# Optimization experiments

Hardware: AMD Instinct MI355X
Metric: run time of the kernel (lower is better)

## Reference

```python
import jax, jax.numpy as jnp
import numpy as np

B, S, HID = 1, 2048, 7168
QLORA = 1536
NH = 32          # index_n_heads
HD = 128         # index_head_dim
ROPE = 64        # qk_rope_head_dim
TOPK = 512       # index_topk
EPS = 1e-6
NEG = -1e9       # finite mask value -> deterministic top-k (no -inf ties)


def _rope(x, cos, sin):
    # non-interleaved rotary: x [b,s,h,d]; cos/sin [s, d//2]
    half = x.shape[-1] // 2
    x1, x2 = x[..., :half], x[..., half:]
    c = cos[None, :, None, :]
    s = sin[None, :, None, :]
    return jnp.concatenate([x1 * c - x2 * s, x1 * s + x2 * c], axis=-1)


def setup_inputs() -> dict:
    key = jax.random.key(0)
    ks = jax.random.split(key, 8)
    x = jax.random.normal(ks[0], (B, S, HID), jnp.float32)
    qr = jax.random.normal(ks[1], (B, S, QLORA), jnp.float32)
    # rotary tables, theta=10000
    inv = 1.0 / (10000.0 ** (np.arange(0, ROPE, 2, dtype=np.float32) / ROPE))
    ang = np.arange(S, dtype=np.float32)[:, None] * inv[None, :]   # [S, ROPE//2]
    freqs_cos = jnp.asarray(np.cos(ang))
    freqs_sin = jnp.asarray(np.sin(ang))
    # causal additive mask [S, S], broadcasts over batch on [b,t,s]
    tri = jnp.tril(jnp.ones((S, S), jnp.bool_))
    mask = jnp.where(tri, 0.0, NEG).astype(jnp.float32)
    wq_b = jax.random.normal(ks[2], (QLORA, NH * HD), jnp.float32) / np.sqrt(QLORA)
    wk = jax.random.normal(ks[3], (HID, HD), jnp.float32) / np.sqrt(HID)
    k_norm_w = jnp.ones((HD,), jnp.float32)
    w_weights = jax.random.normal(ks[4], (HID, NH), jnp.float32) / np.sqrt(HID)
    return {"x": x, "qr": qr, "freqs_cos": freqs_cos, "freqs_sin": freqs_sin,
            "mask": mask, "wq_b": wq_b, "wk": wk, "k_norm_w": k_norm_w,
            "w_weights": w_weights}


def reference(x, qr, freqs_cos, freqs_sin, mask, wq_b, wk, k_norm_w, w_weights):
    b, s, _ = x.shape
    # queries
    q = (qr @ wq_b).reshape(b, s, NH, HD)
    q_pe, q_nope = q[..., :ROPE], q[..., ROPE:]
    q_pe = _rope(q_pe, freqs_cos, freqs_sin)
    q = jnp.concatenate([q_pe, q_nope], axis=-1)            # [b,s,NH,HD]
    # keys: project + RMSNorm + rope on first ROPE dims
    k = x @ wk                                              # [b,s,HD]
    var = jnp.mean(k * k, axis=-1, keepdims=True)
    k = k_norm_w * (k * jax.lax.rsqrt(var + EPS))
    k_pe, k_nope = k[..., :ROPE], k[..., ROPE:]
    k_pe = _rope(k_pe[:, :, None, :], freqs_cos, freqs_sin)[:, :, 0, :]
    k = jnp.concatenate([k_pe, k_nope], axis=-1)            # [b,s,HD]
    # per-head query weights
    weights = (x @ w_weights) * (NH ** -0.5) * (HD ** -0.5)  # [b,s,NH]
    # relu scores and per-head weighted reduction
    logits = jax.nn.relu(jnp.einsum('bthd,bsd->btsh', q, k))  # [b,t,s,NH]
    score = jnp.einsum('btsh,bth->bts', logits, weights) + mask
    # top-k token selection -> additive index mask
    topk_idx = jax.lax.top_k(score, min(TOPK, s))[1]          # [b,t,k]
    bi = jnp.arange(b)[:, None, None]
    ti = jnp.arange(s)[None, :, None]
    out = jnp.full((b, s, s), -jnp.inf, dtype=x.dtype)
    out = out.at[bi, ti, topk_idx].set(0.0)
    return out
```

## Files before the change

kernel.cpp:

```cpp
#include <hip/hip_runtime.h>
#include <hip/hip_bf16.h>
#include <math.h>

#define S_LEN 2048
#define HID   7168
#define QLORA 1536
#define NH    32
#define HD    128
#define T0    512
#define MROWS 1536
#define NEGV  -1000000000.0f
#define EPSV  1e-6f
#define NEG_FILL -3.0e38f
#define KSPLIT 16
#define KCHUNK 448

typedef __attribute__((ext_vector_type(8))) short bf16x8;
typedef __attribute__((ext_vector_type(4))) float f32x4;

__device__ __forceinline__ unsigned short f2bf(float x) {
    __hip_bfloat16 h = __float2bfloat16(x);
    union { __hip_bfloat16 h; unsigned short u; } cv; cv.h = h; return cv.u;
}
__device__ __forceinline__ float bf2f(short u) {
    return __uint_as_float(((unsigned)(unsigned short)u) << 16);
}
__device__ __forceinline__ void gload_lds16(const void* gsrc, void* ldst) {
    __builtin_amdgcn_global_load_lds(
        (const __attribute__((address_space(1))) void*)gsrc,
        (__attribute__((address_space(3))) void*)ldst,
        16, 0, 0);
}

__global__ __launch_bounds__(256) void transpose_wqb(
    const float* __restrict__ B, unsigned short* __restrict__ BT)
{
    __shared__ float tbuf[64][65];
    const int tid = threadIdx.x;
    const int n0 = blockIdx.x * 64;
    const int k0 = blockIdx.y * 64;
    {
        int r = tid >> 2, c0 = (tid & 3) * 16;
        const float* src = &B[(size_t)(k0 + r) * 4096 + n0 + c0];
        #pragma unroll
        for (int i = 0; i < 4; ++i) {
            float4 v = *(const float4*)(src + 4 * i);
            tbuf[r][c0 + 4 * i]     = v.x;
            tbuf[r][c0 + 4 * i + 1] = v.y;
            tbuf[r][c0 + 4 * i + 2] = v.z;
            tbuf[r][c0 + 4 * i + 3] = v.w;
        }
    }
    __syncthreads();
    {
        int nn = tid >> 2, ks = (tid & 3) * 16;
        bf16x8 p0, p1;
        #pragma unroll
        for (int j = 0; j < 8; ++j) {
            p0[j] = (short)f2bf(tbuf[ks + j][nn]);
            p1[j] = (short)f2bf(tbuf[ks + 8 + j][nn]);
        }
        unsigned short* dst = &BT[(size_t)(n0 + nn) * QLORA + k0 + ks];
        *(bf16x8*)dst       = p0;
        *(bf16x8*)(dst + 8) = p1;
    }
}

__global__ __launch_bounds__(256) void transpose_w(
    const float* __restrict__ wk, const float* __restrict__ ww,
    unsigned short* __restrict__ wbT)
{
    __shared__ float tbuf[64][33];
    const int tid = threadIdx.x;
    const int k0 = blockIdx.x * 64;
    const int nt = blockIdx.y;
    const float* src; int ld, nc0;
    if (nt < 4) { src = wk; ld = HD; nc0 = nt * 32; }
    else        { src = ww; ld = NH; nc0 = 0; }
    {
        int r = tid >> 2, c0 = (tid & 3) * 8;
        const float* sp = &src[(size_t)(k0 + r) * ld + nc0 + c0];
        #pragma unroll
        for (int i = 0; i < 2; ++i) {
            float4 v = *(const float4*)(sp + 4 * i);
            tbuf[r][c0 + 4 * i]     = v.x;
            tbuf[r][c0 + 4 * i + 1] = v.y;
            tbuf[r][c0 + 4 * i + 2] = v.z;
            tbuf[r][c0 + 4 * i + 3] = v.w;
        }
    }
    __syncthreads();
    {
        int nn = tid >> 3, ks = (tid & 7) * 8;
        bf16x8 p;
        #pragma unroll
        for (int j = 0; j < 8; ++j) p[j] = (short)f2bf(tbuf[ks + j][nn]);
        *(bf16x8*)&wbT[(size_t)(nt * 32 + nn) * HID + k0 + ks] = p;
    }
}

__global__ __launch_bounds__(256) void cast_qr(
    const float* __restrict__ qr, unsigned short* __restrict__ qrb)
{
    int idx = blockIdx.x * 256 + threadIdx.x;
    const float* src = qr + (size_t)T0 * QLORA + (size_t)idx * 8;
    float4 f0 = *(const float4*)src;
    float4 f1 = *(const float4*)(src + 4);
    bf16x8 p;
    p[0]=(short)f2bf(f0.x); p[1]=(short)f2bf(f0.y); p[2]=(short)f2bf(f0.z); p[3]=(short)f2bf(f0.w);
    p[4]=(short)f2bf(f1.x); p[5]=(short)f2bf(f1.y); p[6]=(short)f2bf(f1.z); p[7]=(short)f2bf(f1.w);
    *(bf16x8*)(qrb + (size_t)idx * 8) = p;
}

__global__ __launch_bounds__(256) void kw_gemm2(
    const float* __restrict__ x, const unsigned short* __restrict__ wbT,
    unsigned short* __restrict__ P)
{
    __shared__ char As[2][4096];
    __shared__ char Bs[2][10240];
    const int tid = threadIdx.x;
    const int bid = blockIdx.x;
    const int wg = (bid & 7) * 64 + (bid >> 3);
    const int kc = wg >> 5;
    const int m0 = (wg & 31) * 64;
    const int kbase = kc * KCHUNK;
    const int wv = tid >> 6, l = tid & 63, g = l >> 4, r15 = l & 15;
    const int ar = tid >> 2, asub = tid & 3;
    f32x4 acc[10] = {};
    float4 fa, fb;

#define LOAD_A(kt) do {                                                          \
        const float* ap = &x[(size_t)(m0 + ar) * HID + kbase + (kt) * 32 + asub * 8]; \
        fa = *(const float4*)ap;  fb = *(const float4*)(ap + 4);                 \
    } while (0)
#define WRITE_A(buf) do {                                                        \
        bf16x8 pk;                                                               \
        pk[0]=(short)f2bf(fa.x); pk[1]=(short)f2bf(fa.y);                        \
        pk[2]=(short)f2bf(fa.z); pk[3]=(short)f2bf(fa.w);                        \
        pk[4]=(short)f2bf(fb.x); pk[5]=(short)f2bf(fb.y);                        \
        pk[6]=(short)f2bf(fb.z); pk[7]=(short)f2bf(fb.w);                        \
        *(bf16x8*)(As[buf] + (ar << 6) + ((asub ^ ((ar >> 1) & 3)) << 4)) = pk;  \
    } while (0)
#define STAGE_B(buf, kt) do {                                                    \
        int k0_ = kbase + (kt) * 32;                                             \
        { int slot = (wv << 6) + l;                                              \
          int n_ = slot >> 2, sub_ = (slot & 3) ^ ((n_ >> 1) & 3);               \
          gload_lds16(wbT + (size_t)n_ * HID + k0_ + sub_ * 8,                   \
                      Bs[buf] + (wv << 10)); }                                   \
        { int slot = 256 + (wv << 6) + l;                                        \
          int n_ = slot >> 2, sub_ = (slot & 3) ^ ((n_ >> 1) & 3);               \
          gload_lds16(wbT + (size_t)n_ * HID + k0_ + sub_ * 8,                   \
                      Bs[buf] + 4096 + (wv << 10)); }                            \
        if (wv < 2) {                                                            \
          int slot = 512 + (wv << 6) + l;                                        \
          int n_ = slot >> 2, sub_ = (slot & 3) ^ ((n_ >> 1) & 3);               \
          gload_lds16(wbT + (size_t)n_ * HID + k0_ + sub_ * 8,                   \
                      Bs[buf] + 8192 + (wv << 10)); }                            \
    } while (0)

    LOAD_A(0);
    STAGE_B(0, 0);
    WRITE_A(0);
    __syncthreads();
    int cur = 0;
    for (int t = 0; t < 14; ++t) {
        if (t < 13) { LOAD_A(t + 1); STAGE_B(cur ^ 1, t + 1); }
        {
            char* Ab = As[cur];
            char* Bb = Bs[cur];
            int ra = (wv << 4) + r15;
            bf16x8 a = *(const bf16x8*)(Ab + (ra << 6) + ((g ^ ((ra >> 1) & 3)) << 4));
            #pragma unroll
            for (int fn = 0; fn < 10; ++fn) {
                int nb = (fn << 4) + r15;
                bf16x8 b = *(const bf16x8*)(Bb + (nb << 6) + ((g ^ ((nb >> 1) & 3)) << 4));
                acc[fn] = __builtin_amdgcn_mfma_f32_16x16x32_bf16(a, b, acc[fn], 0, 0, 0);
            }
        }
        if (t < 13) WRITE_A(cur ^ 1);
        __syncthreads();
        cur ^= 1;
    }
#undef LOAD_A
#undef WRITE_A
#undef STAGE_B
    #pragma unroll
    for (int fn = 0; fn < 10; ++fn)
        #pragma unroll
        for (int rr = 0; rr < 4; ++rr) {
            int row = m0 + (wv << 4) + (g << 2) + rr;
            P[((size_t)kc * S_LEN + row) * 160 + (fn << 4) + r15] = f2bf(acc[fn][rr]);
        }
}

__global__ __launch_bounds__(512) void kw_finish16(
    const unsigned short* __restrict__ P, const float* __restrict__ knw,
    const float* __restrict__ fcos, const float* __restrict__ fsin,
    unsigned short* __restrict__ Kf, float* __restrict__ W)
{
    __shared__ float res[16][160];
    __shared__ float rsq[16];
    const int tid = threadIdx.x;
    const int stile = blockIdx.x;
    const int row0 = stile * 16;
    const int r = tid >> 5, j = tid & 31;

    #pragma unroll
    for (int jj = 0; jj < 5; ++jj) {
        int c = j + 32 * jj;
        float s = 0.f;
        #pragma unroll
        for (int kc = 0; kc < KSPLIT; ++kc)
            s += bf2f((short)P[(size_t)(kc * S_LEN + row0 + r) * 160 + c]);
        res[r][c] = s;
    }
    __syncthreads();
    {
        float s2 = 0.f;
        #pragma unroll
        for (int cg = 0; cg < 4; ++cg) { float v = res[r][cg * 32 + j]; s2 += v * v; }
        #pragma unroll
        for (int off = 16; off > 0; off >>= 1) s2 += __shfl_xor(s2, off, 32);
        if (j == 0) rsq[r] = rsqrtf(s2 * (1.0f / 128.0f) + EPSV);
    }
    __syncthreads();
    {
        int rr = tid >> 5, h = tid & 31;
        W[(size_t)(row0 + rr) * NH + h] = res[rr][128 + h] * 0.015625f;
    }
    if (tid < 256) {
        int ks = tid >> 6, l = tid & 63;
        int row = l & 15, g = l >> 4;
        int t = row0 + row;
        float rs = rsq[row];
        bf16x8 pack;
        #pragma unroll
        for (int jj2 = 0; jj2 < 8; ++jj2) {
            int d = ks * 32 + 8 * g + jj2;
            float v;
            if (d < 32) {
                float a = res[row][d]      * rs * knw[d];
                float b = res[row][d + 32] * rs * knw[d + 32];
                v = a * fcos[(size_t)t * 32 + d] - b * fsin[(size_t)t * 32 + d];
            } else if (d < 64) {
                int jx = d - 32;
                float a = res[row][jx] * rs * knw[jx];
                float b = res[row][d]  * rs * knw[d];
                v = a * fsin[(size_t)t * 32 + jx] + b * fcos[(size_t)t * 32 + jx];
            } else {
                v = res[row][d] * rs * knw[d];
            }
            pack[jj2] = (short)f2bf(v);
        }
        *(bf16x8*)&Kf[(size_t)stile * 2048 + ks * 512 + l * 8] = pack;
    }
}

__global__ __launch_bounds__(256) void gemm_q2(
    const unsigned short* __restrict__ qrb, const unsigned short* __restrict__ wqbT,
    const float* __restrict__ fcos, const float* __restrict__ fsin,
    unsigned short* __restrict__ Qbu)
{
    __shared__ char lds[2][12288];
    const int tid = threadIdx.x;
    const int bid = blockIdx.x;
    const int wg = (bid & 7) * 96 + (bid >> 3);
    const int n0 = (wg / 24) * 128;
    const int m0 = (wg % 24) * 64;
    const int wv = tid >> 6, l = tid & 63, g = l >> 4, r15 = l & 15;
    const int lrow = l >> 2, lsub = l & 3;
    const int wm = wv >> 1, wn = wv & 1;
    f32x4 acc[2][4] = {};

#define STAGE_Q(buf, kt) do {                                                   \
        int k0_ = (kt) * 32;                                                    \
        { int row_ = wv * 16 + lrow; int gs_ = lsub ^ ((row_ >> 1) & 3);        \
          gload_lds16(qrb + (size_t)(m0 + row_) * QLORA + k0_ + gs_ * 8,        \
                      lds[buf] + (wv << 10)); }                                 \
        { int row_ = wv * 32 + lrow; int gs_ = lsub ^ ((row_ >> 1) & 3);        \
          gload_lds16(wqbT + (size_t)(n0 + row_) * QLORA + k0_ + gs_ * 8,       \
                      lds[buf] + 4096 + (wv << 11)); }                          \
        { int row_ = wv * 32 + 16 + lrow; int gs_ = lsub ^ ((row_ >> 1) & 3);   \
          gload_lds16(wqbT + (size_t)(n0 + row_) * QLORA + k0_ + gs_ * 8,       \
                      lds[buf] + 4096 + (wv << 11) + 1024); }                   \
    } while (0)

    STAGE_Q(0, 0);
    __syncthreads();
    int cur = 0;
    for (int t = 0; t < 48; ++t) {
        if (t + 1 < 48) STAGE_Q(cur ^ 1, t + 1);
        char* As = lds[cur];
        char* Bs = lds[cur] + 4096;
        bf16x8 a[2], b[4];
        #pragma unroll
        for (int fm = 0; fm < 2; ++fm) {
            int ra = wm * 32 + fm * 16 + r15;
            a[fm] = *(const bf16x8*)(As + (ra << 6) + ((g ^ ((ra >> 1) & 3)) << 4));
        }
        #pragma unroll
        for (int fn = 0; fn < 4; ++fn) {
            int nb = wn * 64 + fn * 16 + r15;
            b[fn] = *(const bf16x8*)(Bs + (nb << 6) + ((g ^ ((nb >> 1) & 3)) << 4));
        }
        #pragma unroll
        for (int fm = 0; fm < 2; ++fm)
            #pragma unroll
            for (int fn = 0; fn < 4; ++fn)
                acc[fm][fn] = __builtin_amdgcn_mfma_f32_16x16x32_bf16(a[fm], b[fn], acc[fm][fn], 0, 0, 0);
        __syncthreads();
        cur ^= 1;
    }
#undef STAGE_Q
    if (wn == 0) {
        #pragma unroll
        for (int fm = 0; fm < 2; ++fm)
            #pragma unroll
            for (int rr = 0; rr < 4; ++rr) {
                int t = T0 + m0 + wm * 32 + fm * 16 + 4 * g + rr;
                #pragma unroll
                for (int p = 0; p < 2; ++p) {
                    int jj = p * 16 + r15;
                    float c = fcos[(size_t)t * 32 + jj];
                    float s = fsin[(size_t)t * 32 + jj];
                    float a = acc[fm][p][rr], b = acc[fm][p + 2][rr];
                    acc[fm][p][rr]     = a * c - b * s;
                    acc[fm][p + 2][rr] = a * s + b * c;
                }
            }
    }
    #pragma unroll
    for (int fm = 0; fm < 2; ++fm)
        #pragma unroll
        for (int fn = 0; fn < 4; ++fn)
            #pragma unroll
            for (int rr = 0; rr < 4; ++rr) {
                int row = m0 + wm * 32 + fm * 16 + 4 * g + rr;
                int col = n0 + wn * 64 + fn * 16 + r15;
                Qbu[(size_t)row * 4096 + col] = f2bf(acc[fm][fn][rr]);
            }
}

__global__ __launch_bounds__(256, 2) void score_mfma2(
    const unsigned short* __restrict__ Qb, const unsigned short* __restrict__ Kf,
    const float* __restrict__ W, float* __restrict__ sc)
{
    __shared__ float ps[4][320];
    __shared__ float wl2[32][16];
    const int tid = threadIdx.x;
    const int tt  = 95 - blockIdx.x;
    const int sp  = blockIdx.y;
    const int t0  = T0 + 16 * tt;
    const int wv  = tid >> 6, l = tid & 63, g = l >> 4, r15 = l & 15;

    for (int i = tid; i < 512; i += 256) {
        int h = i >> 4, gg = (i >> 2) & 3, r = i & 3;
        wl2[h][gg * 4 + r] = W[(size_t)(t0 + 4 * gg + r) * NH + h];
    }
    bf16x8 qf[8][4];
    {
        const unsigned short* qbase = Qb + (size_t)(16 * tt + r15) * 4096 + g * 8;
        #pragma unroll
        for (int hh = 0; hh < 8; ++hh)
            #pragma unroll
            for (int ks = 0; ks < 4; ++ks)
                qf[hh][ks] = *(const bf16x8*)(qbase + (8 * wv + hh) * 128 + ks * 32);
    }
    __syncthreads();

    const int nst = 33 + tt;
    for (int stile = sp; stile < nst; stile += 4) {
        bf16x8 kf[4];
        #pragma unroll
        for (int ks = 0; ks < 4; ++ks)
            kf[ks] = *(const bf16x8*)&Kf[(size_t)stile * 2048 + ks * 512 + l * 8];
        f32x4 score = {0.f, 0.f, 0.f, 0.f};
        #pragma unroll
        for (int hh = 0; hh < 8; ++hh) {
            f32x4 acc = {0.f, 0.f, 0.f, 0.f};
            #pragma unroll
            for (int ks = 0; ks < 4; ++ks)
                acc = __builtin_amdgcn_mfma_f32_16x16x32_bf16(qf[hh][ks], kf[ks], acc, 0, 0, 0);
            f32x4 w4 = *(const f32x4*)&wl2[8 * wv + hh][g * 4];
            #pragma unroll
            for (int r = 0; r < 4; ++r)
                score[r] += fmaxf(acc[r], 0.f) * w4[r];
        }
        #pragma unroll
        for (int r = 0; r < 4; ++r) ps[wv][l * 5 + r] = score[r];
        __syncthreads();
        {
            float v = ((ps[0][l * 5 + wv] + ps[1][l * 5 + wv])
                       + ps[2][l * 5 + wv]) + ps[3][l * 5 + wv];
            int t = t0 + 4 * g + wv;
            int s = stile * 16 + r15;
            sc[(size_t)(t - T0) * S_LEN + s] = (s <= t) ? v : NEGV;
        }
        __syncthreads();
    }
}

__global__ __launch_bounds__(256) void topk_row(
    const float* __restrict__ sc, float* __restrict__ out)
{
    __shared__ float scl[S_LEN];
    __shared__ unsigned int hist[256];
    __shared__ unsigned int wtot[4];
    __shared__ unsigned int sh_prefix;
    __shared__ int sh_krem;
    const int tid = threadIdx.x;
    const int lane = tid & 63, wvi = tid >> 6;
    const int qrow = blockIdx.x;
    const int t = T0 + qrow;
    const float* srow = sc + (size_t)qrow * S_LEN;

    for (int i = tid; i < S_LEN; i += 256) {
        float v = srow[i];
        scl[i] = (i <= t) ? v : NEGV;
    }
    __syncthreads();
    unsigned int* u = (unsigned int*)scl;
    #pragma unroll
    for (int jj = 0; jj < 8; ++jj) {
        int i = tid * 8 + jj;
        unsigned int b = __float_as_uint(scl[i]);
        u[i] = (b & 0x80000000u) ? ~b : (b | 0x80000000u);
    }
    if (tid == 0) { sh_prefix = 0u; sh_krem = 512; }
    __syncthreads();

    #pragma unroll
    for (int pass = 0; pass < 4; ++pass) {
        const int shift = 24 - 8 * pass;
        hist[tid] = 0u;
        __syncthreads();
        unsigned int pfx = sh_prefix;
        #pragma unroll
        for (int jj = 0; jj < 8; ++jj) {
            unsigned int uv = u[tid * 8 + jj];
            bool ok = (pass == 0) || ((uv >> (shift + 8)) == (pfx >> (shift + 8)));
            if (ok) atomicAdd(&hist[(uv >> shift) & 255u], 1u);
        }
        __syncthreads();
        unsigned int v = hist[tid];
        unsigned int s = v;
        #pragma unroll
        for (int off = 1; off < 64; off <<= 1) {
            unsigned int t2 = __shfl_down(s, off, 64);
            if (lane + off < 64) s += t2;
        }
        if (lane == 0) wtot[wvi] = s;
        int krem = sh_krem;
        __syncthreads();
        unsigned int S = s;
        #pragma unroll
        for (int w = 0; w < 4; ++w)
            if (w > wvi) S += wtot[w];
        if ((int)S >= krem && (int)(S - v) < krem) {
            sh_krem = krem - (int)(S - v);
            sh_prefix = pfx | ((unsigned int)tid << shift);
        }
        __syncthreads();
    }

    const unsigned int uthr = sh_prefix;
    const int krem = sh_krem;
    int ec = 0;
    #pragma unroll
    for (int jj = 0; jj < 8; ++jj) ec += (u[tid * 8 + jj] == uthr) ? 1 : 0;
    unsigned int c = (unsigned int)ec;
    unsigned int p = c;
    #pragma unroll
    for (int off = 1; off < 64; off <<= 1) {
        unsigned int t2 = __shfl_up(p, off, 64);
        if (lane >= off) p += t2;
    }
    if (lane == 63) wtot[wvi] = p;
    __syncthreads();
    unsigned int add = 0;
    #pragma unroll
    for (int w = 0; w < 4; ++w)
        if (w < wvi) add += wtot[w];
    int base = (int)(p - c + add);

    float* orow = out + (size_t)t * S_LEN;
    float o[8];
    #pragma unroll
    for (int jj = 0; jj < 8; ++jj) {
        unsigned int uv = u[tid * 8 + jj];
        bool sel;
        if (uv > uthr) { sel = true; }
        else if (uv == uthr) { sel = (base < krem); base++; }
        else { sel = false; }
        o[jj] = sel ? 0.0f : NEG_FILL;
    }
    float4 o0 = {o[0], o[1], o[2], o[3]};
    float4 o1 = {o[4], o[5], o[6], o[7]};
    *(float4*)&orow[tid * 8]     = o0;
    *(float4*)&orow[tid * 8 + 4] = o1;
}

__global__ __launch_bounds__(256) void fill_low(float* __restrict__ out)
{
    int idx = blockIdx.x * 256 + threadIdx.x;
    if (idx >= (T0 * S_LEN) / 4) return;
    int col4 = idx & 511;
    float v = (col4 < 128) ? 0.0f : NEG_FILL;
    float4 o = {v, v, v, v};
    ((float4*)out)[idx] = o;
}

extern "C" void kernel_launch(void* const* d_in, const int* in_sizes, int n_in,
                              void* d_out, int out_size, void* d_ws, size_t ws_size,
                              hipStream_t stream)
{
    (void)in_sizes; (void)n_in; (void)out_size; (void)ws_size;
    const float* x    = (const float*)d_in[0];
    const float* qr   = (const float*)d_in[1];
    const float* fcos = (const float*)d_in[2];
    const float* fsin = (const float*)d_in[3];
    const float* wq_b = (const float*)d_in[5];
    const float* wk   = (const float*)d_in[6];
    const float* knw  = (const float*)d_in[7];
    const float* ww   = (const float*)d_in[8];
    float* out = (float*)d_out;
    char*  wsb = (char*)d_ws;

    unsigned short* Kf   = (unsigned short*)wsb;
    float*          W    = (float*)(wsb + 512 * 1024);
    char*           reg1 = wsb + 768 * 1024;
    char*           reg2 = reg1 + 12582912;
    unsigned short* wbT  = (unsigned short*)reg1;
    unsigned short* Qbu  = (unsigned short*)reg1;
    unsigned short* P    = (unsigned short*)reg2;
    unsigned short* wqbT = (unsigned short*)reg2;
    float*          sc   = (float*)reg2;
    unsigned short* qrb  = (unsigned short*)d_out;

    transpose_w   <<<dim3(112, 5), 256, 0, stream>>>(wk, ww, wbT);
    kw_gemm2      <<<512, 256,        0, stream>>>(x, wbT, P);
    kw_finish16   <<<128, 512,        0, stream>>>(P, knw, fcos, fsin, Kf, W);
    transpose_wqb <<<dim3(64, 24), 256, 0, stream>>>(wq_b, wqbT);
    cast_qr       <<<1152, 256,       0, stream>>>(qr, qrb);
    gemm_q2       <<<768, 256,        0, stream>>>(qrb, wqbT, fcos, fsin, Qbu);
    score_mfma2   <<<dim3(96, 4), 256,  0, stream>>>(Qbu, Kf, W, sc);
    topk_row      <<<MROWS, 256,      0, stream>>>(sc, out);
    fill_low      <<<(T0 * S_LEN / 4 + 255) / 256, 256, 0, stream>>>(out);
}
```

Measured before the change: 159.3 us.

## Split score kernel heads across 8 waves with K prefetch and double-buffered reduction

The score kernel now runs 512 threads per block, so each wave handles 4 heads instead of 8, which halves the Q fragment registers held per thread. K fragments for the next s-tile are prefetched while the current tile's MFMAs run. The partial-sum buffer is double-buffered so the trailing barrier can be dropped. In exchange the cross-wave reduction sums 8 partials instead of 4, and only half the waves do the final reduce and store.

Measured after the change: 156.0 us. 1.02x faster.

```diff
diff --git a/kernel.cpp b/kernel.cpp
--- a/kernel.cpp
+++ b/kernel.cpp
@@ -341,11 +341,11 @@
             }
 }
 
-__global__ __launch_bounds__(256, 2) void score_mfma2(
+__global__ __launch_bounds__(512, 2) void score_mfma3(
     const unsigned short* __restrict__ Qb, const unsigned short* __restrict__ Kf,
     const float* __restrict__ W, float* __restrict__ sc)
 {
-    __shared__ float ps[4][320];
+    __shared__ float ps[2][8][320];
     __shared__ float wl2[32][16];
     const int tid = threadIdx.x;
     const int tt  = 95 - blockIdx.x;
@@ -353,50 +353,61 @@
     const int t0  = T0 + 16 * tt;
     const int wv  = tid >> 6, l = tid & 63, g = l >> 4, r15 = l & 15;
 
-    for (int i = tid; i < 512; i += 256) {
-        int h = i >> 4, gg = (i >> 2) & 3, r = i & 3;
+    {
+        int h = tid >> 4, gg = (tid >> 2) & 3, r = tid & 3;
         wl2[h][gg * 4 + r] = W[(size_t)(t0 + 4 * gg + r) * NH + h];
     }
-    bf16x8 qf[8][4];
+    bf16x8 qf[4][4];
     {
         const unsigned short* qbase = Qb + (size_t)(16 * tt + r15) * 4096 + g * 8;
         #pragma unroll
-        for (int hh = 0; hh < 8; ++hh)
+        for (int hh = 0; hh < 4; ++hh)
             #pragma unroll
             for (int ks = 0; ks < 4; ++ks)
-                qf[hh][ks] = *(const bf16x8*)(qbase + (8 * wv + hh) * 128 + ks * 32);
+                qf[hh][ks] = *(const bf16x8*)(qbase + (4 * wv + hh) * 128 + ks * 32);
     }
     __syncthreads();
 
     const int nst = 33 + tt;
+    bf16x8 kfc[4], kfn[4];
+    if (sp < nst) {
+        #pragma unroll
+        for (int ks = 0; ks < 4; ++ks)
+            kfc[ks] = *(const bf16x8*)&Kf[(size_t)sp * 2048 + ks * 512 + l * 8];
+    }
+    int pb = 0;
     for (int stile = sp; stile < nst; stile += 4) {
-        bf16x8 kf[4];
-        #pragma unroll
-        for (int ks = 0; ks < 4; ++ks)
-            kf[ks] = *(const bf16x8*)&Kf[(size_t)stile * 2048 + ks * 512 + l * 8];
+        if (stile + 4 < nst) {
+            #pragma unroll
+            for (int ks = 0; ks < 4; ++ks)
+                kfn[ks] = *(const bf16x8*)&Kf[(size_t)(stile + 4) * 2048 + ks * 512 + l * 8];
+        }
         f32x4 score = {0.f, 0.f, 0.f, 0.f};
         #pragma unroll
-        for (int hh = 0; hh < 8; ++hh) {
+        for (int hh = 0; hh < 4; ++hh) {
             f32x4 acc = {0.f, 0.f, 0.f, 0.f};
             #pragma unroll
             for (int ks = 0; ks < 4; ++ks)
-                acc = __builtin_amdgcn_mfma_f32_16x16x32_bf16(qf[hh][ks], kf[ks], acc, 0, 0, 0);
-            f32x4 w4 = *(const f32x4*)&wl2[8 * wv + hh][g * 4];
+                acc = __builtin_amdgcn_mfma_f32_16x16x32_bf16(qf[hh][ks], kfc[ks], acc, 0, 0, 0);
+            f32x4 w4 = *(const f32x4*)&wl2[4 * wv + hh][g * 4];
             #pragma unroll
             for (int r = 0; r < 4; ++r)
                 score[r] += fmaxf(acc[r], 0.f) * w4[r];
         }
         #pragma unroll
-        for (int r = 0; r < 4; ++r) ps[wv][l * 5 + r] = score[r];
-        __syncthreads();
-        {
-            float v = ((ps[0][l * 5 + wv] + ps[1][l * 5 + wv])
-                       + ps[2][l * 5 + wv]) + ps[3][l * 5 + wv];
+        for (int r = 0; r < 4; ++r) ps[pb][wv][l * 5 + r] = score[r];
+        __syncthreads();
+        if (wv < 4) {
+            float v = ps[pb][0][l * 5 + wv];
+            #pragma unroll
+            for (int w = 1; w < 8; ++w) v += ps[pb][w][l * 5 + wv];
             int t = t0 + 4 * g + wv;
             int s = stile * 16 + r15;
             sc[(size_t)(t - T0) * S_LEN + s] = (s <= t) ? v : NEGV;
         }
-        __syncthreads();
+        #pragma unroll
+        for (int ks = 0; ks < 4; ++ks) kfc[ks] = kfn[ks];
+        pb ^= 1;
     }
 }
 
@@ -543,7 +554,7 @@
     transpose_wqb <<<dim3(64, 24), 256, 0, stream>>>(wq_b, wqbT);
     cast_qr       <<<1152, 256,       0, stream>>>(qr, qrb);
     gemm_q2       <<<768, 256,        0, stream>>>(qrb, wqbT, fcos, fsin, Qbu);
-    score_mfma2   <<<dim3(96, 4), 256,  0, stream>>>(Qbu, Kf, W, sc);
+    score_mfma3   <<<dim3(96, 4), 512,  0, stream>>>(Qbu, Kf, W, sc);
     topk_row      <<<MROWS, 256,      0, stream>>>(sc, out);
     fill_low      <<<(T0 * S_LEN / 4 + 255) / 256, 256, 0, stream>>>(out);
 }
```
